# Performance work log

Hardware: AMD Instinct MI355X
Metric: run time of the kernel (lower is better)

Reference implementation:

```python
import jax, jax.numpy as jnp
import numpy as np

B, T, C, H = 4, 2048, 1024, 16
D = C // H  # head dim = 64
ROPE_BASE = 10000.0


def _rope_cache(seq_len, dim, dtype=jnp.float32):
    # torchtune-style interleaved RoPE cache
    inv_freq = 1.0 / (ROPE_BASE ** (jnp.arange(0, dim, 2, dtype=jnp.float32) / dim))
    t = jnp.arange(seq_len, dtype=jnp.float32)
    freqs = jnp.outer(t, inv_freq)  # [T, D/2]
    return jnp.cos(freqs).astype(dtype), jnp.sin(freqs).astype(dtype)


def _apply_rope(x, cos, sin):
    # x: [B, H, T, D]; rotate interleaved pairs along last dim
    x1 = x[..., 0::2]
    x2 = x[..., 1::2]
    # broadcast cos/sin [T, D/2] -> [1, 1, T, D/2]
    o1 = x1 * cos - x2 * sin
    o2 = x2 * cos + x1 * sin
    out = jnp.stack([o1, o2], axis=-1).reshape(x.shape)
    return out


def setup_inputs() -> dict:
    key = jax.random.key(0)
    k1, k2, k3 = jax.random.split(key, 3)
    x = jax.random.normal(k1, (B, T, C), dtype=jnp.float32)
    W_in = jax.random.normal(k2, (C, 3 * C), dtype=jnp.float32) * (1.0 / np.sqrt(C))
    b_in = jnp.zeros((3 * C,), dtype=jnp.float32)
    W_out = jax.random.normal(k3, (C, C), dtype=jnp.float32) * (1.0 / np.sqrt(C))
    b_out = jnp.zeros((C,), dtype=jnp.float32)
    return {"x": x, "W_in": W_in, "b_in": b_in, "W_out": W_out, "b_out": b_out}


def reference(x, W_in, b_in, W_out, b_out):
    Bx, Tx, Cx = x.shape
    qkv = x @ W_in + b_in                      # [B, T, 3C]
    q, k, v = jnp.split(qkv, 3, axis=-1)
    # [B, T, C] -> [B, H, T, D]
    def to_heads(t):
        return t.reshape(Bx, Tx, H, D).transpose(0, 2, 1, 3)
    q, k, v = to_heads(q), to_heads(k), to_heads(v)

    cos, sin = _rope_cache(Tx, D, dtype=x.dtype)
    q = _apply_rope(q, cos, sin)
    k = _apply_rope(k, cos, sin)

    scale = 1.0 / np.sqrt(D)
    att = jnp.einsum('bhqd,bhkd->bhqk', q, k) * scale   # [B, H, T, T]
    causal = jnp.tril(jnp.ones((Tx, Tx), dtype=bool))
    att = jnp.where(causal[None, None, :, :], att, jnp.float32(-jnp.inf).astype(att.dtype))
    att = jax.nn.softmax(att, axis=-1)
    # dropout = 0.0 (eval mode): identity
    y = jnp.einsum('bhqk,bhkd->bhqd', att, v)           # [B, H, T, D]
    y = y.transpose(0, 2, 1, 3).reshape(Bx, Tx, Cx)     # [B, T, C]
    return y @ W_out + b_out
```

## Files before the change

### kernel.cpp

```cpp
#include <hip/hip_runtime.h>

#define B_ 4
#define T_ 2048
#define C_ 1024
#define H_ 16
#define D_ 64
#define M_ (B_*T_)
#define N3_ (3*C_)
#define NKT_ 32

typedef unsigned short u16;
typedef short bf16x8 __attribute__((ext_vector_type(8)));
typedef short bf16x4 __attribute__((ext_vector_type(4)));
typedef unsigned short u16x8 __attribute__((ext_vector_type(8)));
typedef unsigned int u32x4 __attribute__((ext_vector_type(4)));
typedef float f32x4 __attribute__((ext_vector_type(4)));
typedef float f32x16 __attribute__((ext_vector_type(16)));

#define QSCALE 0.18033688f
#define DEFER_THR 11.0f

__device__ __forceinline__ u16 f2bf(float f) {
  unsigned u = __float_as_uint(f);
  u += 0x7fffu + ((u >> 16) & 1u);
  return (u16)(u >> 16);
}

__device__ __forceinline__ unsigned cvt_pk_bf16(float lo, float hi) {
  unsigned r;
  asm("v_cvt_pk_bf16_f32 %0, %1, %2" : "=v"(r) : "v"(lo), "v"(hi));
  return r;
}

__device__ __forceinline__ void gload16(const void* g, void* l) {
  __builtin_amdgcn_global_load_lds((const __attribute__((address_space(1))) void*)g,
                                   (__attribute__((address_space(3))) void*)l, 16, 0, 0);
}

__device__ __forceinline__ int epi_key(int ml) { return (ml ^ (ml >> 3)) & 7; }

__global__ __launch_bounds__(256) void k_prep(const float* __restrict__ x,
                                              u16* __restrict__ xbf,
                                              const float* __restrict__ W_in,
                                              u16* __restrict__ WtIn,
                                              const float* __restrict__ W_out,
                                              u16* __restrict__ WtOut,
                                              float* __restrict__ ct,
                                              float* __restrict__ st) {
  __shared__ float tile[64][65];
  const int bx = blockIdx.x, tid = threadIdx.x;
  if (bx < 4096) {
    int i = bx * 256 + tid;
    f32x4 a = *(const f32x4*)(x + (size_t)i * 8);
    f32x4 b = *(const f32x4*)(x + (size_t)i * 8 + 4);
    u16x8 o;
    #pragma unroll
    for (int j = 0; j < 4; ++j) { o[j] = f2bf(a[j]); o[4 + j] = f2bf(b[j]); }
    *(u16x8*)(xbf + (size_t)i * 8) = o;
  } else if (bx < 5120) {
    const float* W; u16* Wt; int K = C_, N, b;
    if (bx < 4864) { W = W_in; Wt = WtIn; N = N3_; b = bx - 4096; }
    else           { W = W_out; Wt = WtOut; N = C_; b = bx - 4864; }
    int ntiles = N / 64;
    int n0 = (b % ntiles) * 64, k0 = (b / ntiles) * 64;
    int c = tid & 63, r0 = tid >> 6;
    #pragma unroll
    for (int i = 0; i < 16; ++i) {
      int r = i * 4 + r0;
      tile[r][c] = W[(size_t)(k0 + r) * N + n0 + c];
    }
    __syncthreads();
    #pragma unroll
    for (int i = 0; i < 16; ++i) {
      int r = i * 4 + r0;
      Wt[(size_t)(n0 + r) * K + k0 + c] = f2bf(tile[c][r]);
    }
  } else {
    int idx = (bx - 5120) * 256 + tid;
    int t = idx >> 5, i = idx & 31;
    double inv = exp(-(2.0 * (double)i / 64.0) * log(10000.0));
    double a = (double)t * inv;
    ct[idx] = (float)cos(a);
    st[idx] = (float)sin(a);
  }
}

template <int MODE>
__global__ __launch_bounds__(256) void k_gemm(const u16* __restrict__ A,
                                              const u16* __restrict__ Bt,
                                              const float* __restrict__ bias,
                                              float* __restrict__ Cout,
                                              u16* __restrict__ Qb, u16* __restrict__ Kb,
                                              u16* __restrict__ Vt,
                                              const float* __restrict__ ctab,
                                              const float* __restrict__ stab,
                                              int Md, int Nd, int Kd) {
  __shared__ u16 sA[128 * 128];
  __shared__ u16 sB[128 * 128];
  const int tid = threadIdx.x, lane = tid & 63, w = tid >> 6;
  const int g = lane >> 4, r = lane & 15;
  const int wm = w >> 1, wn = w & 1;
  const int lin = blockIdx.y * gridDim.x + blockIdx.x;
  const int tM = ((lin & 7) * 8 + ((lin >> 3) & 7)) * 128;
  const int tN = (lin >> 6) * 128;

  f32x4 acc[4][4];
  #pragma unroll
  for (int i = 0; i < 4; ++i)
    #pragma unroll
    for (int j = 0; j < 4; ++j) acc[i][j] = (f32x4){0.f, 0.f, 0.f, 0.f};

  for (int k0 = 0; k0 < Kd; k0 += 128) {
    #pragma unroll
    for (int i = 0; i < 8; ++i) {
      int c = i * 256 + tid, row = c >> 4, slot = (c & 15) ^ (row & 15);
      gload16(A + (size_t)(tM + row) * Kd + k0 + slot * 8, sA + (i * 256 + w * 64) * 8);
    }
    #pragma unroll
    for (int i = 0; i < 8; ++i) {
      int c = i * 256 + tid, row = c >> 4, slot = (c & 15) ^ (row & 15);
      gload16(Bt + (size_t)(tN + row) * Kd + k0 + slot * 8, sB + (i * 256 + w * 64) * 8);
    }
    __syncthreads();
    #pragma unroll
    for (int kk = 0; kk < 4; ++kk) {
      bf16x8 af[4], bfr[4];
      #pragma unroll
      for (int mt = 0; mt < 4; ++mt) {
        int row = wm * 64 + mt * 16 + r;
        af[mt] = *(const bf16x8*)(sA + row * 128 + (((kk * 4 + g) ^ (row & 15)) * 8));
      }
      #pragma unroll
      for (int nt = 0; nt < 4; ++nt) {
        int row = wn * 64 + nt * 16 + r;
        bfr[nt] = *(const bf16x8*)(sB + row * 128 + (((kk * 4 + g) ^ (row & 15)) * 8));
      }
      __builtin_amdgcn_s_setprio(1);
      #pragma unroll
      for (int mt = 0; mt < 4; ++mt)
        #pragma unroll
        for (int nt = 0; nt < 4; ++nt)
          acc[mt][nt] = __builtin_amdgcn_mfma_f32_16x16x32_bf16(af[mt], bfr[nt],
                                                                acc[mt][nt], 0, 0, 0);
      __builtin_amdgcn_s_setprio(0);
    }
    __syncthreads();
  }

  if (MODE == 1) {
    #pragma unroll
    for (int mt = 0; mt < 4; ++mt)
      #pragma unroll
      for (int nt = 0; nt < 4; ++nt) {
        int n = tN + wn * 64 + nt * 16 + r;
        float bv = bias[n];
        #pragma unroll
        for (int reg = 0; reg < 4; ++reg) {
          int m = tM + wm * 64 + mt * 16 + g * 4 + reg;
          Cout[(size_t)m * Nd + n] = acc[mt][nt][reg] + bv;
        }
      }
  } else {
    const int secb = tN >> 10;
    u16* tile = sA;
    #pragma unroll
    for (int mt = 0; mt < 4; ++mt)
      #pragma unroll
      for (int nt = 0; nt < 4; ++nt) {
        int nl = wn * 64 + nt * 16 + r;
        int n = tN + nl;
        float bv = bias[n];
        int dd = n & 63;
        #pragma unroll
        for (int reg = 0; reg < 4; ++reg) {
          int ml = wm * 64 + mt * 16 + g * 4 + reg;
          int tt = (tM + ml) & (T_ - 1);
          float v = acc[mt][nt][reg] + bv;
          if (secb < 2) {
            float pv = __shfl_xor(v, 1);
            int pi = tt * 32 + (dd >> 1);
            float c = ctab[pi], sn = stab[pi];
            v = (dd & 1) ? (v * c + pv * sn) : (v * c - pv * sn);
            if (secb == 0) v *= QSCALE;
          }
          tile[ml * 128 + ((((nl >> 3) ^ epi_key(ml)) << 3) | (nl & 7))] = f2bf(v);
        }
      }
    __syncthreads();
    if (secb < 2) {
      u16* dst = secb == 0 ? Qb : Kb;
      #pragma unroll
      for (int i = 0; i < 8; ++i) {
        int row = w * 32 + (i & 3) * 8 + (lane >> 3);
        int cc = (i >> 2) * 8 + (lane & 7);
        u16x8 val = *(const u16x8*)(tile + row * 128 + ((cc ^ epi_key(row)) << 3));
        int n = tN + cc * 8;
        int m = tM + row;
        int hh = (n & 1023) >> 6, dd = n & 63;
        int bb = m >> 11, tt = m & (T_ - 1);
        *(u16x8*)(dst + ((size_t)(bb * H_ + hh) * T_ + tt) * D_ + dd) = val;
      }
    } else {
      const int bb = tM >> 11, tt0 = tM & (T_ - 1);
      #pragma unroll
      for (int v = 0; v < 8; ++v) {
        int idx = v * 256 + tid;
        int nl = idx >> 4;
        int tg = idx & 15;
        u16x8 val;
        #pragma unroll
        for (int j = 0; j < 8; ++j) {
          int ml = tg * 8 + j;
          val[j] = tile[ml * 128 + ((((nl >> 3) ^ epi_key(ml)) << 3) | (nl & 7))];
        }
        int n = tN + nl;
        int hh = (n & 1023) >> 6, dd = n & 63;
        *(u16x8*)(Vt + ((size_t)(bb * H_ + hh) * D_ + dd) * T_ + tt0 + tg * 8) = val;
      }
    }
  }
}

__global__ __launch_bounds__(128) void k_attn(const u16* __restrict__ Qb,
                                              const u16* __restrict__ Kb,
                                              const u16* __restrict__ Vt,
                                              u16* __restrict__ Y) {
  __shared__ u16 sK[2][64 * 64];
  __shared__ u16 sV[2][64 * 64];
  const int tid = threadIdx.x, w = tid >> 6;
  const int lane = tid & 63, col = lane & 31, hi = lane >> 5;
  const int pair = blockIdx.x;
  const int h = blockIdx.y, b = blockIdx.z;
  const size_t bhK = ((size_t)b * H_ + h) * T_;
  const size_t bhV = ((size_t)b * H_ + h) * D_;

  const int qtA = pair, qtB = (NKT_ - 1) - pair;
  const int ntA = qtA + 1;
  const int total = NKT_ + 1;

  auto STAGE = [&](int buf, int kt) {
    #pragma unroll
    for (int i = 0; i < 4; ++i) {
      int c = i * 128 + tid, row = c >> 3, slot = (c & 7) ^ (row & 7);
      gload16(Kb + (bhK + kt * 64 + row) * D_ + slot * 8, &sK[buf][(i * 128 + w * 64) * 8]);
    }
    #pragma unroll
    for (int i = 0; i < 4; ++i) {
      int c = i * 128 + tid, row = c >> 3, slot = (c & 7) ^ (row & 7);
      gload16(Vt + (bhV + row) * T_ + kt * 64 + slot * 8, &sV[buf][(i * 128 + w * 64) * 8]);
    }
  };

  int qw = qtA * 64 + w * 32;
  int tq = qw + col;
  bf16x8 qf[4];
  #pragma unroll
  for (int c = 0; c < 4; ++c)
    qf[c] = *(const bf16x8*)(Qb + (bhK + tq) * D_ + c * 16 + hi * 8);

  float m_run = -3e38f, l_run = 0.f;
  f32x16 o0, o1;
  #pragma unroll
  for (int i = 0; i < 16; ++i) { o0[i] = 0.f; o1[i] = 0.f; }

  auto FINAL = [&]() {
    float lr = l_run + __shfl_xor(l_run, 32);
    float rl = 1.0f / lr;
    u16* yrow = Y + ((size_t)b * T_ + tq) * C_ + h * 64;
    #pragma unroll
    for (int dt = 0; dt < 2; ++dt)
      #pragma unroll
      for (int j = 0; j < 8; ++j) {
        float a0 = (dt ? o1[2 * j] : o0[2 * j]) * rl;
        float a1 = (dt ? o1[2 * j + 1] : o0[2 * j + 1]) * rl;
        int d = dt * 32 + 8 * (j >> 1) + 4 * hi + 2 * (j & 1);
        *(unsigned*)(yrow + d) = cvt_pk_bf16(a0, a1);
      }
  };

  STAGE(0, 0);
  __syncthreads();

  for (int it = 0; it < total; ++it) {
    const int cur = it & 1;
    if (it + 1 < total) {
      int nit = it + 1;
      STAGE(cur ^ 1, nit < ntA ? nit : nit - ntA);
    }
    const int ktl = it < ntA ? it : it - ntA;
    const int kb = ktl * 64;
    if (kb <= qw + 31) {
      const bool act1 = (kb + 32 <= qw + 31);
      f32x16 s0, s1;
      #pragma unroll
      for (int i = 0; i < 16; ++i) { s0[i] = 0.f; s1[i] = 0.f; }

      __builtin_amdgcn_s_setprio(1);
      #pragma unroll
      for (int c = 0; c < 4; ++c) {
        int row = col;
        bf16x8 kf = *(const bf16x8*)(&sK[cur][(row * 64 + c * 16 + hi * 8) ^ ((row & 7) << 3)]);
        s0 = __builtin_amdgcn_mfma_f32_32x32x16_bf16(kf, qf[c], s0, 0, 0, 0);
      }
      if (act1) {
        #pragma unroll
        for (int c = 0; c < 4; ++c) {
          int row = 32 + col;
          bf16x8 kf = *(const bf16x8*)(&sK[cur][(row * 64 + c * 16 + hi * 8) ^ ((row & 7) << 3)]);
          s1 = __builtin_amdgcn_mfma_f32_32x32x16_bf16(kf, qf[c], s1, 0, 0, 0);
        }
      }
      __builtin_amdgcn_s_setprio(0);

      if (kb + 31 > qw) {
        #pragma unroll
        for (int reg = 0; reg < 16; ++reg) {
          int key = kb + (reg & 3) + 8 * (reg >> 2) + 4 * hi;
          if (key > tq) s0[reg] = -3e38f;
        }
      }
      if (act1 && kb + 63 > qw) {
        #pragma unroll
        for (int reg = 0; reg < 16; ++reg) {
          int key = kb + 32 + (reg & 3) + 8 * (reg >> 2) + 4 * hi;
          if (key > tq) s1[reg] = -3e38f;
        }
      }

      float pm = s0[0];
      #pragma unroll
      for (int reg = 1; reg < 16; ++reg) pm = fmaxf(pm, s0[reg]);
      if (act1) {
        #pragma unroll
        for (int reg = 0; reg < 16; ++reg) pm = fmaxf(pm, s1[reg]);
      }
      if (__any(pm > m_run + DEFER_THR)) {
        float tm = fmaxf(pm, __shfl_xor(pm, 32));
        float mn = fmaxf(m_run, tm);
        float f = __builtin_amdgcn_exp2f(m_run - mn);
        m_run = mn;
        #pragma unroll
        for (int i = 0; i < 16; ++i) { o0[i] *= f; o1[i] *= f; }
        l_run *= f;
      }

      #pragma unroll
      for (int reg = 0; reg < 16; ++reg) {
        s0[reg] = __builtin_amdgcn_exp2f(s0[reg] - m_run);
        l_run += s0[reg];
      }
      if (act1) {
        #pragma unroll
        for (int reg = 0; reg < 16; ++reg) {
          s1[reg] = __builtin_amdgcn_exp2f(s1[reg] - m_run);
          l_run += s1[reg];
        }
      }

      __builtin_amdgcn_s_setprio(1);
      #pragma unroll
      for (int st = 0; st < 2; ++st) {
        if (st == 1 && !act1) break;
        #pragma unroll
        for (int u = 0; u < 2; ++u) {
          u32x4 pw;
          #pragma unroll
          for (int j = 0; j < 4; ++j) {
            int jr = (4 * u + j) * 2;
            pw[j] = st ? cvt_pk_bf16(s1[jr], s1[jr + 1])
                       : cvt_pk_bf16(s0[jr], s0[jr + 1]);
          }
          bf16x8 pf = __builtin_bit_cast(bf16x8, pw);
          const int keybase = st * 32 + u * 16;
          #pragma unroll
          for (int dt = 0; dt < 2; ++dt) {
            int row = dt * 32 + col;
            int e0 = (row * 64 + keybase + 4 * hi) ^ ((row & 7) << 3);
            int e1 = (row * 64 + keybase + 8 + 4 * hi) ^ ((row & 7) << 3);
            bf16x4 vlo = *(const bf16x4*)(&sV[cur][e0]);
            bf16x4 vhi = *(const bf16x4*)(&sV[cur][e1]);
            bf16x8 vf;
            vf[0] = vlo[0]; vf[1] = vlo[1]; vf[2] = vlo[2]; vf[3] = vlo[3];
            vf[4] = vhi[0]; vf[5] = vhi[1]; vf[6] = vhi[2]; vf[7] = vhi[3];
            if (dt == 0) o0 = __builtin_amdgcn_mfma_f32_32x32x16_bf16(vf, pf, o0, 0, 0, 0);
            else         o1 = __builtin_amdgcn_mfma_f32_32x32x16_bf16(vf, pf, o1, 0, 0, 0);
          }
        }
      }
      __builtin_amdgcn_s_setprio(0);
    }
    __syncthreads();

    if (it == ntA - 1) {
      FINAL();
      qw = qtB * 64 + w * 32;
      tq = qw + col;
      #pragma unroll
      for (int c = 0; c < 4; ++c)
        qf[c] = *(const bf16x8*)(Qb + (bhK + tq) * D_ + c * 16 + hi * 8);
      m_run = -3e38f; l_run = 0.f;
      #pragma unroll
      for (int i = 0; i < 16; ++i) { o0[i] = 0.f; o1[i] = 0.f; }
    }
  }
  FINAL();
}

extern "C" void kernel_launch(void* const* d_in, const int* in_sizes, int n_in,
                              void* d_out, int out_size, void* d_ws, size_t ws_size,
                              hipStream_t stream) {
  const float* x     = (const float*)d_in[0];
  const float* W_in  = (const float*)d_in[1];
  const float* b_in  = (const float*)d_in[2];
  const float* W_out = (const float*)d_in[3];
  const float* b_out = (const float*)d_in[4];
  float* out = (float*)d_out;

  const size_t NE = (size_t)B_ * H_ * T_ * D_;
  u16* Qb    = (u16*)d_ws;
  u16* Kb    = Qb + NE;
  u16* Vt    = Kb + NE;
  u16* xbf   = Vt + NE;
  u16* WtIn  = xbf + (size_t)M_ * C_;
  u16* WtOut = WtIn + (size_t)N3_ * C_;
  float* ctab = (float*)(WtOut + (size_t)C_ * C_);
  float* stab = ctab + T_ * 32;
  u16* ybf = xbf;

  size_t needed = (size_t)((char*)(stab + T_ * 32) - (char*)d_ws);
  if (ws_size < needed) return;

  k_prep<<<5376, 256, 0, stream>>>(x, xbf, W_in, WtIn, W_out, WtOut, ctab, stab);

  k_gemm<0><<<dim3(N3_ / 128, M_ / 128), 256, 0, stream>>>(
      xbf, WtIn, b_in, nullptr, Qb, Kb, Vt, ctab, stab, M_, N3_, C_);

  k_attn<<<dim3(NKT_ / 2, H_, B_), 128, 0, stream>>>(Qb, Kb, Vt, ybf);

  k_gemm<1><<<dim3(C_ / 128, M_ / 128), 256, 0, stream>>>(
      ybf, WtOut, b_out, out, nullptr, nullptr, nullptr, nullptr, nullptr, M_, C_, C_);
}
```

Measured before the change: 198.6 us.

## Retile GEMM to 256x128 blocks with K-step 64 and split epilogue

The bf16 GEMM block tile changes from 128x128 with K-step 128 to 256x128 with K-step 64. Each wave now owns a 64x128 sub-tile with 32 accumulators, and the epilogue writes through LDS in two 128-row halves. The aim is more MFMA work per LDS fragment load and fewer blocks, trading for higher register pressure and half as many workgroups. With fewer blocks, CU utilisation may drop, especially for the output projection (256 blocks).

```diff
diff --git a/kernel.cpp b/kernel.cpp
--- a/kernel.cpp
+++ b/kernel.cpp
@@ -95,51 +95,50 @@
                                               const float* __restrict__ ctab,
                                               const float* __restrict__ stab,
                                               int Md, int Nd, int Kd) {
-  __shared__ u16 sA[128 * 128];
-  __shared__ u16 sB[128 * 128];
+  __shared__ u16 sA[256 * 64];
+  __shared__ u16 sB[128 * 64];
   const int tid = threadIdx.x, lane = tid & 63, w = tid >> 6;
   const int g = lane >> 4, r = lane & 15;
-  const int wm = w >> 1, wn = w & 1;
   const int lin = blockIdx.y * gridDim.x + blockIdx.x;
-  const int tM = ((lin & 7) * 8 + ((lin >> 3) & 7)) * 128;
-  const int tN = (lin >> 6) * 128;
-
-  f32x4 acc[4][4];
+  const int tM = ((lin & 7) * 4 + ((lin >> 3) & 3)) * 256;
+  const int tN = (lin >> 5) * 128;
+
+  f32x4 acc[4][8];
   #pragma unroll
   for (int i = 0; i < 4; ++i)
     #pragma unroll
-    for (int j = 0; j < 4; ++j) acc[i][j] = (f32x4){0.f, 0.f, 0.f, 0.f};
-
-  for (int k0 = 0; k0 < Kd; k0 += 128) {
+    for (int j = 0; j < 8; ++j) acc[i][j] = (f32x4){0.f, 0.f, 0.f, 0.f};
+
+  for (int k0 = 0; k0 < Kd; k0 += 64) {
     #pragma unroll
     for (int i = 0; i < 8; ++i) {
-      int c = i * 256 + tid, row = c >> 4, slot = (c & 15) ^ (row & 15);
+      int c = i * 256 + tid, row = c >> 3, slot = (c & 7) ^ (row & 7);
       gload16(A + (size_t)(tM + row) * Kd + k0 + slot * 8, sA + (i * 256 + w * 64) * 8);
     }
     #pragma unroll
-    for (int i = 0; i < 8; ++i) {
-      int c = i * 256 + tid, row = c >> 4, slot = (c & 15) ^ (row & 15);
+    for (int i = 0; i < 4; ++i) {
+      int c = i * 256 + tid, row = c >> 3, slot = (c & 7) ^ (row & 7);
       gload16(Bt + (size_t)(tN + row) * Kd + k0 + slot * 8, sB + (i * 256 + w * 64) * 8);
     }
     __syncthreads();
     #pragma unroll
-    for (int kk = 0; kk < 4; ++kk) {
-      bf16x8 af[4], bfr[4];
+    for (int kk = 0; kk < 2; ++kk) {
+      bf16x8 af[4], bfr[8];
       #pragma unroll
       for (int mt = 0; mt < 4; ++mt) {
-        int row = wm * 64 + mt * 16 + r;
-        af[mt] = *(const bf16x8*)(sA + row * 128 + (((kk * 4 + g) ^ (row & 15)) * 8));
-      }
-      #pragma unroll
-      for (int nt = 0; nt < 4; ++nt) {
-        int row = wn * 64 + nt * 16 + r;
-        bfr[nt] = *(const bf16x8*)(sB + row * 128 + (((kk * 4 + g) ^ (row & 15)) * 8));
+        int row = w * 64 + mt * 16 + r;
+        af[mt] = *(const bf16x8*)(sA + ((row * 64 + kk * 32 + g * 8) ^ ((row & 7) << 3)));
+      }
+      #pragma unroll
+      for (int nt = 0; nt < 8; ++nt) {
+        int row = nt * 16 + r;
+        bfr[nt] = *(const bf16x8*)(sB + ((row * 64 + kk * 32 + g * 8) ^ ((row & 7) << 3)));
       }
       __builtin_amdgcn_s_setprio(1);
       #pragma unroll
       for (int mt = 0; mt < 4; ++mt)
         #pragma unroll
-        for (int nt = 0; nt < 4; ++nt)
+        for (int nt = 0; nt < 8; ++nt)
           acc[mt][nt] = __builtin_amdgcn_mfma_f32_16x16x32_bf16(af[mt], bfr[nt],
                                                                 acc[mt][nt], 0, 0, 0);
       __builtin_amdgcn_s_setprio(0);
@@ -151,72 +150,79 @@
     #pragma unroll
     for (int mt = 0; mt < 4; ++mt)
       #pragma unroll
-      for (int nt = 0; nt < 4; ++nt) {
-        int n = tN + wn * 64 + nt * 16 + r;
+      for (int nt = 0; nt < 8; ++nt) {
+        int n = tN + nt * 16 + r;
         float bv = bias[n];
         #pragma unroll
         for (int reg = 0; reg < 4; ++reg) {
-          int m = tM + wm * 64 + mt * 16 + g * 4 + reg;
+          int m = tM + w * 64 + mt * 16 + g * 4 + reg;
           Cout[(size_t)m * Nd + n] = acc[mt][nt][reg] + bv;
         }
       }
   } else {
     const int secb = tN >> 10;
     u16* tile = sA;
-    #pragma unroll
-    for (int mt = 0; mt < 4; ++mt)
-      #pragma unroll
-      for (int nt = 0; nt < 4; ++nt) {
-        int nl = wn * 64 + nt * 16 + r;
-        int n = tN + nl;
-        float bv = bias[n];
-        int dd = n & 63;
-        #pragma unroll
-        for (int reg = 0; reg < 4; ++reg) {
-          int ml = wm * 64 + mt * 16 + g * 4 + reg;
-          int tt = (tM + ml) & (T_ - 1);
-          float v = acc[mt][nt][reg] + bv;
-          if (secb < 2) {
-            float pv = __shfl_xor(v, 1);
-            int pi = tt * 32 + (dd >> 1);
-            float c = ctab[pi], sn = stab[pi];
-            v = (dd & 1) ? (v * c + pv * sn) : (v * c - pv * sn);
-            if (secb == 0) v *= QSCALE;
+    const int bb = tM >> 11;
+    #pragma unroll
+    for (int half = 0; half < 2; ++half) {
+      if ((w >> 1) == half) {
+        #pragma unroll
+        for (int mt = 0; mt < 4; ++mt)
+          #pragma unroll
+          for (int nt = 0; nt < 8; ++nt) {
+            int nl = nt * 16 + r;
+            int n = tN + nl;
+            float bv = bias[n];
+            int dd = n & 63;
+            #pragma unroll
+            for (int reg = 0; reg < 4; ++reg) {
+              int lrow = (w & 1) * 64 + mt * 16 + g * 4 + reg;
+              int tt = (tM + half * 128 + lrow) & (T_ - 1);
+              float v = acc[mt][nt][reg] + bv;
+              if (secb < 2) {
+                float pv = __shfl_xor(v, 1);
+                int pi = tt * 32 + (dd >> 1);
+                float c = ctab[pi], sn = stab[pi];
+                v = (dd & 1) ? (v * c + pv * sn) : (v * c - pv * sn);
+                if (secb == 0) v *= QSCALE;
+              }
+              tile[lrow * 128 + ((((nl >> 3) ^ epi_key(lrow)) << 3) | (nl & 7))] = f2bf(v);
+            }
           }
-          tile[ml * 128 + ((((nl >> 3) ^ epi_key(ml)) << 3) | (nl & 7))] = f2bf(v);
-        }
-      }
-    __syncthreads();
-    if (secb < 2) {
-      u16* dst = secb == 0 ? Qb : Kb;
-      #pragma unroll
-      for (int i = 0; i < 8; ++i) {
-        int row = w * 32 + (i & 3) * 8 + (lane >> 3);
-        int cc = (i >> 2) * 8 + (lane & 7);
-        u16x8 val = *(const u16x8*)(tile + row * 128 + ((cc ^ epi_key(row)) << 3));
-        int n = tN + cc * 8;
-        int m = tM + row;
-        int hh = (n & 1023) >> 6, dd = n & 63;
-        int bb = m >> 11, tt = m & (T_ - 1);
-        *(u16x8*)(dst + ((size_t)(bb * H_ + hh) * T_ + tt) * D_ + dd) = val;
-      }
-    } else {
-      const int bb = tM >> 11, tt0 = tM & (T_ - 1);
-      #pragma unroll
-      for (int v = 0; v < 8; ++v) {
-        int idx = v * 256 + tid;
-        int nl = idx >> 4;
-        int tg = idx & 15;
-        u16x8 val;
-        #pragma unroll
-        for (int j = 0; j < 8; ++j) {
-          int ml = tg * 8 + j;
-          val[j] = tile[ml * 128 + ((((nl >> 3) ^ epi_key(ml)) << 3) | (nl & 7))];
-        }
-        int n = tN + nl;
-        int hh = (n & 1023) >> 6, dd = n & 63;
-        *(u16x8*)(Vt + ((size_t)(bb * H_ + hh) * D_ + dd) * T_ + tt0 + tg * 8) = val;
-      }
+      }
+      __syncthreads();
+      if (secb < 2) {
+        u16* dst = secb == 0 ? Qb : Kb;
+        #pragma unroll
+        for (int i = 0; i < 8; ++i) {
+          int row = w * 32 + (i & 3) * 8 + (lane >> 3);
+          int cc = (i >> 2) * 8 + (lane & 7);
+          u16x8 val = *(const u16x8*)(tile + row * 128 + ((cc ^ epi_key(row)) << 3));
+          int n = tN + cc * 8;
+          int m = tM + half * 128 + row;
+          int hh = (n & 1023) >> 6, dd = n & 63;
+          int tt = m & (T_ - 1);
+          *(u16x8*)(dst + ((size_t)(bb * H_ + hh) * T_ + tt) * D_ + dd) = val;
+        }
+      } else {
+        const int tt0 = (tM + half * 128) & (T_ - 1);
+        #pragma unroll
+        for (int v = 0; v < 8; ++v) {
+          int idx = v * 256 + tid;
+          int nl = idx >> 4;
+          int tg = idx & 15;
+          u16x8 val;
+          #pragma unroll
+          for (int j = 0; j < 8; ++j) {
+            int ml = tg * 8 + j;
+            val[j] = tile[ml * 128 + ((((nl >> 3) ^ epi_key(ml)) << 3) | (nl & 7))];
+          }
+          int n = tN + nl;
+          int hh = (n & 1023) >> 6, dd = n & 63;
+          *(u16x8*)(Vt + ((size_t)(bb * H_ + hh) * D_ + dd) * T_ + tt0 + tg * 8) = val;
+        }
+      }
+      __syncthreads();
     }
   }
 }
@@ -432,11 +438,11 @@
 
   k_prep<<<5376, 256, 0, stream>>>(x, xbf, W_in, WtIn, W_out, WtOut, ctab, stab);
 
-  k_gemm<0><<<dim3(N3_ / 128, M_ / 128), 256, 0, stream>>>(
+  k_gemm<0><<<dim3(N3_ / 128, M_ / 256), 256, 0, stream>>>(
       xbf, WtIn, b_in, nullptr, Qb, Kb, Vt, ctab, stab, M_, N3_, C_);
 
   k_attn<<<dim3(NKT_ / 2, H_, B_), 128, 0, stream>>>(Qb, Kb, Vt, ybf);
 
-  k_gemm<1><<<dim3(C_ / 128, M_ / 128), 256, 0, stream>>>(
+  k_gemm<1><<<dim3(C_ / 128, M_ / 256), 256, 0, stream>>>(
       ybf, WtOut, b_out, out, nullptr, nullptr, nullptr, nullptr, nullptr, M_, C_, C_);
 }
```

Result: slower. 365.0 us (+83.8%).
